# Performance work log

Hardware: AMD Instinct MI355X
Metric: run time of the kernel (lower is better)

Reference implementation:

```python
import jax, jax.numpy as jnp
import numpy as np


def gru_cell(x, h, Wih, Whh, bih, bhh):
    # torch GRU cell, gate order r, z, n
    gi = x @ Wih.T + bih
    gh = h @ Whh.T + bhh
    ir, iz, inn = jnp.split(gi, 3, axis=-1)
    hr, hz, hn = jnp.split(gh, 3, axis=-1)
    r = jax.nn.sigmoid(ir + hr)
    z = jax.nn.sigmoid(iz + hz)
    n = jnp.tanh(inn + r * hn)
    return (1.0 - z) * n + z * h


def setup_inputs() -> dict:
    key = jax.random.key(0)
    ks = jax.random.split(key, 24)
    S, T, B, E, H, V = 64, 64, 32, 512, 1024, 32000
    sc_e = 1.0 / np.sqrt(E)
    sc_h = 1.0 / np.sqrt(H)

    def rn(i, shape, sc):
        return jax.random.normal(ks[i], shape, jnp.float32) * sc

    return {
        "src": jax.random.randint(ks[0], (S, B), 0, V),
        "trg": jax.random.randint(ks[1], (T, B), 0, V),
        "emb": rn(2, (V, E), 0.02),
        # encoder forward-direction GRU
        "Wih_f": rn(3, (3 * H, E), sc_e), "Whh_f": rn(4, (3 * H, H), sc_h),
        "bih_f": rn(5, (3 * H,), sc_h), "bhh_f": rn(6, (3 * H,), sc_h),
        # encoder backward-direction GRU
        "Wih_b": rn(7, (3 * H, E), sc_e), "Whh_b": rn(8, (3 * H, H), sc_h),
        "bih_b": rn(9, (3 * H,), sc_h), "bhh_b": rn(10, (3 * H,), sc_h),
        # attention: Linear(2H -> H) and scoring vector v
        "Wa": rn(11, (H, 2 * H), sc_h), "ba": rn(12, (H,), sc_h),
        "v": rn(13, (H,), sc_h),
        # decoder GRU: input is [embedded(E); context(H)]
        "Wih_d": rn(14, (3 * H, E + H), sc_h), "Whh_d": rn(15, (3 * H, H), sc_h),
        "bih_d": rn(16, (3 * H,), sc_h), "bhh_d": rn(17, (3 * H,), sc_h),
        # output head Linear(2H -> V)
        "Wout": rn(18, (V, 2 * H), sc_h), "bout": rn(19, (V,), sc_h),
    }


def reference(src, trg, emb, Wih_f, Whh_f, bih_f, bhh_f, Wih_b, Whh_b, bih_b, bhh_b,
              Wa, ba, v, Wih_d, Whh_d, bih_d, bhh_d, Wout, bout):
    S, B = src.shape
    H = Whh_f.shape[1]

    # ---- encoder: bidirectional GRU, fwd+bwd output halves summed ----
    src_emb = emb[src]  # [S, B, E]
    h0 = jnp.zeros((B, H), src_emb.dtype)

    def step_f(h, x):
        h2 = gru_cell(x, h, Wih_f, Whh_f, bih_f, bhh_f)
        return h2, h2

    def step_b(h, x):
        h2 = gru_cell(x, h, Wih_b, Whh_b, bih_b, bhh_b)
        return h2, h2

    h_fwd, out_f = jax.lax.scan(step_f, h0, src_emb)
    _, out_b_rev = jax.lax.scan(step_b, h0, src_emb[::-1])
    enc_out = out_f + out_b_rev[::-1]          # [S, B, H]
    enc_bt = enc_out.transpose(1, 0, 2)        # [B, S, H]

    # ---- decoder with teacher forcing (ratio fixed to 1.0) ----
    dec_tokens = jnp.concatenate([src[-1:], trg[:-1]], axis=0)  # [T, B]
    dec_emb = emb[dec_tokens]                                   # [T, B, E]

    def dec_step(h, e_t):
        # Bahdanau attention: relu(Linear([h; enc])) scored by v
        hrep = jnp.broadcast_to(h[:, None, :], enc_bt.shape)    # [B, S, H]
        energy = jax.nn.relu(jnp.concatenate([hrep, enc_bt], -1) @ Wa.T + ba)
        scores = energy @ v                                     # [B, S]
        a = jax.nn.softmax(scores, axis=1)
        ctx = jnp.einsum('bs,bsh->bh', a, enc_bt)               # [B, H]
        rnn_in = jnp.concatenate([e_t, ctx], axis=-1)           # [B, E+H]
        h_new = gru_cell(rnn_in, h, Wih_d, Whh_d, bih_d, bhh_d)
        logits = jnp.concatenate([h_new, ctx], -1) @ Wout.T + bout  # [B, V]
        return h_new, logits

    _, outputs = jax.lax.scan(dec_step, h_fwd, dec_emb)  # [T, B, V]
    return outputs
```

## Files before the change

kernel.cpp:

```cpp
#include <hip/hip_runtime.h>
#include <hip/hip_bf16.h>

#define S_ 64
#define T_ 64
#define B_ 32
#define E_ 512
#define H_ 1024
#define V_ 32000
#define H3 3072
#define H2 2048
#define EH 1536

typedef unsigned short u16;
typedef unsigned int u32;
typedef unsigned long long u64;
typedef __attribute__((ext_vector_type(8))) short bf16x8;
typedef __attribute__((ext_vector_type(4))) float f32x4;

#define MFMA3(ACC, AH_, AL_, BH_, BL_)                                              \
    ACC = __builtin_amdgcn_mfma_f32_16x16x32_bf16(AL_, BH_, ACC, 0, 0, 0);          \
    ACC = __builtin_amdgcn_mfma_f32_16x16x32_bf16(AH_, BL_, ACC, 0, 0, 0);          \
    ACC = __builtin_amdgcn_mfma_f32_16x16x32_bf16(AH_, BH_, ACC, 0, 0, 0);

__device__ __forceinline__ void splitf(float x, u16& h, u16& l) {
    u32 xb = __float_as_uint(x);
    u32 hb = (xb + 0x7FFFu + ((xb >> 16) & 1u)) & 0xFFFF0000u;
    h = (u16)(hb >> 16);
    float lf = x - __uint_as_float(hb);
    u32 lb = __float_as_uint(lf);
    l = (u16)((lb + 0x7FFFu + ((lb >> 16) & 1u)) >> 16);
}

__device__ __forceinline__ float bf2f(u16 v) { return __uint_as_float(((u32)v) << 16); }

__device__ __forceinline__ void load_lds16(const void* g, void* l) {
    __builtin_amdgcn_global_load_lds((const __attribute__((address_space(1))) u32*)g,
                                     (__attribute__((address_space(3))) u32*)l, 16, 0, 0);
}

__device__ __forceinline__ bf16x8 ld_sys16(const u16* p) {
    union { bf16x8 v; u64 q[2]; } u;
    const u64* q = (const u64*)p;
    u.q[0] = __hip_atomic_load(q,     __ATOMIC_RELAXED, __HIP_MEMORY_SCOPE_SYSTEM);
    u.q[1] = __hip_atomic_load(q + 1, __ATOMIC_RELAXED, __HIP_MEMORY_SCOPE_SYSTEM);
    return u.v;
}
__device__ __forceinline__ float ld_sysf(const float* p) {
    return __hip_atomic_load(p, __ATOMIC_RELAXED, __HIP_MEMORY_SCOPE_SYSTEM);
}
__device__ __forceinline__ void st_sysf(float* p, float v) {
    __hip_atomic_store(p, v, __ATOMIC_RELAXED, __HIP_MEMORY_SCOPE_SYSTEM);
}
__device__ __forceinline__ void st_sysu16(u16* p, u16 v) {
    __hip_atomic_store(p, v, __ATOMIC_RELAXED, __HIP_MEMORY_SCOPE_SYSTEM);
}

__device__ __forceinline__ void gbar(int* cnt, int* flag, int nblk, int blk, int& gen) {
    __syncthreads();
    if (threadIdx.x == 0) {
        gen += 1;
        asm volatile("s_waitcnt vmcnt(0)" ::: "memory");
        __hip_atomic_fetch_add(&cnt[(blk & 7) << 5], 1, __ATOMIC_RELAXED,
                               __HIP_MEMORY_SCOPE_SYSTEM);
        if (blk == 0) {
            const int target = nblk * gen;
            for (;;) {
                int sum = 0;
#pragma unroll
                for (int j = 0; j < 8; ++j)
                    sum += __hip_atomic_load(&cnt[j << 5], __ATOMIC_RELAXED,
                                             __HIP_MEMORY_SCOPE_SYSTEM);
                if (sum >= target) break;
                __builtin_amdgcn_s_sleep(2);
            }
#pragma unroll
            for (int j = 0; j < 8; ++j)
                __hip_atomic_store(&flag[j << 5], gen, __ATOMIC_RELAXED,
                                   __HIP_MEMORY_SCOPE_SYSTEM);
        } else {
            while (__hip_atomic_load(&flag[(blk & 7) << 5], __ATOMIC_RELAXED,
                                     __HIP_MEMORY_SCOPE_SYSTEM) < gen)
                __builtin_amdgcn_s_sleep(2);
        }
    }
    __syncthreads();
}

__global__ void k_embed_src_split(const int* __restrict__ src, const float* __restrict__ emb,
                                  u16* __restrict__ hi, u16* __restrict__ lo) {
    int row = blockIdx.x;
    int tok = src[row];
    int c = threadIdx.x * 4;
    float4 v = *reinterpret_cast<const float4*>(emb + (size_t)tok * E_ + c);
    ushort4 h, l;
    splitf(v.x, h.x, l.x); splitf(v.y, h.y, l.y);
    splitf(v.z, h.z, l.z); splitf(v.w, h.w, l.w);
    *reinterpret_cast<ushort4*>(hi + (size_t)row * E_ + c) = h;
    *reinterpret_cast<ushort4*>(lo + (size_t)row * E_ + c) = l;
}

__global__ void k_embed_dec_split(const int* __restrict__ src, const int* __restrict__ trg,
                                  const float* __restrict__ emb,
                                  u16* __restrict__ hi, u16* __restrict__ lo) {
    int row = blockIdx.x;
    int t = row >> 5, b = row & 31;
    int tok = (t == 0) ? src[(S_ - 1) * B_ + b] : trg[(t - 1) * B_ + b];
    int c = threadIdx.x * 4;
    float4 v = *reinterpret_cast<const float4*>(emb + (size_t)tok * E_ + c);
    ushort4 h, l;
    splitf(v.x, h.x, l.x); splitf(v.y, h.y, l.y);
    splitf(v.z, h.z, l.z); splitf(v.w, h.w, l.w);
    *reinterpret_cast<ushort4*>(hi + (size_t)row * E_ + c) = h;
    *reinterpret_cast<ushort4*>(lo + (size_t)row * E_ + c) = l;
}

__global__ __launch_bounds__(256) void k_split(const float* __restrict__ in, int ld, int cols4,
                                               u16* __restrict__ hi, u16* __restrict__ lo) {
    int c4 = blockIdx.x * 256 + threadIdx.x;
    if (c4 >= cols4) return;
    size_t r = blockIdx.y;
    float4 v = *reinterpret_cast<const float4*>(in + r * ld + (size_t)c4 * 4);
    ushort4 h, l;
    splitf(v.x, h.x, l.x); splitf(v.y, h.y, l.y);
    splitf(v.z, h.z, l.z); splitf(v.w, h.w, l.w);
    size_t o = (r * cols4 + c4) * 4;
    *reinterpret_cast<ushort4*>(hi + o) = h;
    *reinterpret_cast<ushort4*>(lo + o) = l;
}

__global__ __launch_bounds__(256) void k_split_sum_enc(
    const float* __restrict__ ef, const float* __restrict__ eb, float* __restrict__ es,
    u16* __restrict__ hi, u16* __restrict__ lo) {
    size_t r = blockIdx.y;
    int c4 = threadIdx.x * 4;
    float4 va = *reinterpret_cast<const float4*>(ef + r * H_ + c4);
    float4 vb = *reinterpret_cast<const float4*>(eb + r * H_ + c4);
    float4 v; v.x = va.x + vb.x; v.y = va.y + vb.y; v.z = va.z + vb.z; v.w = va.w + vb.w;
    *reinterpret_cast<float4*>(es + r * H_ + c4) = v;
    ushort4 h, l;
    splitf(v.x, h.x, l.x); splitf(v.y, h.y, l.y);
    splitf(v.z, h.z, l.z); splitf(v.w, h.w, l.w);
    *reinterpret_cast<ushort4*>(hi + r * H_ + c4) = h;
    *reinterpret_cast<ushort4*>(lo + r * H_ + c4) = l;
}

__global__ void k_wsplit_perm(const float* __restrict__ src, int ld, int coff,
                              u16* __restrict__ hi, u16* __restrict__ lo) {
    int r = blockIdx.x;
    int i = r / 3, g = r - i * 3;
    const float* p = src + (size_t)(g * H_ + i) * ld + coff;
    int c = threadIdx.x * 4;
    float4 v = *reinterpret_cast<const float4*>(p + c);
    ushort4 h, l;
    splitf(v.x, h.x, l.x); splitf(v.y, h.y, l.y);
    splitf(v.z, h.z, l.z); splitf(v.w, h.w, l.w);
    *reinterpret_cast<ushort4*>(hi + (size_t)r * H_ + c) = h;
    *reinterpret_cast<ushort4*>(lo + (size_t)r * H_ + c) = l;
}

__global__ __launch_bounds__(256, 2) void k_gemm_mfma3(
    const u16* __restrict__ Ah, const u16* __restrict__ Al,
    const u16* __restrict__ Bh, const u16* __restrict__ Bl,
    const float* __restrict__ bias, float* __restrict__ C,
    int ldc, int K)
{
    __shared__ u16 ls[4][128 * 32];
    const int tid = threadIdx.x;
    const int lane = tid & 63, w = tid >> 6;
    const int wr = w >> 1, wc = w & 1;
    const size_t m0 = (size_t)blockIdx.x * 128, n0 = (size_t)blockIdx.y * 128;

    const int c0 = (w * 2) * 64 + lane;
    const int r0 = c0 >> 2, kc0 = (c0 & 3) << 3;
    const size_t rstep = (size_t)16 * K;
    const u16* gAh = Ah + (m0 + r0) * K + kc0;
    const u16* gAl = Al + (m0 + r0) * K + kc0;
    const u16* gBh = Bh + (n0 + r0) * K + kc0;
    const u16* gBl = Bl + (n0 + r0) * K + kc0;
    const int lo0 = c0 * 8;

    const int frow = lane & 15, fk = (lane >> 4) << 3;
    const int offA = (wr * 64 + frow) * 32 + fk;
    const int offB = (wc * 64 + frow) * 32 + fk;

    f32x4 acc[4][4] = {};

    for (int k0 = 0; k0 < K; k0 += 32) {
        load_lds16(gAh + k0, &ls[0][lo0]);
        load_lds16(gAh + rstep + k0, &ls[0][lo0 + 512]);
        load_lds16(gAl + k0, &ls[1][lo0]);
        load_lds16(gAl + rstep + k0, &ls[1][lo0 + 512]);
        load_lds16(gBh + k0, &ls[2][lo0]);
        load_lds16(gBh + rstep + k0, &ls[2][lo0 + 512]);
        load_lds16(gBl + k0, &ls[3][lo0]);
        load_lds16(gBl + rstep + k0, &ls[3][lo0 + 512]);
        __syncthreads();

        bf16x8 fAh[4], fAl[4], fBh[4], fBl[4];
#pragma unroll
        for (int m = 0; m < 4; ++m) {
            fAh[m] = *reinterpret_cast<const bf16x8*>(&ls[0][offA + m * 512]);
            fAl[m] = *reinterpret_cast<const bf16x8*>(&ls[1][offA + m * 512]);
        }
#pragma unroll
        for (int n = 0; n < 4; ++n) {
            fBh[n] = *reinterpret_cast<const bf16x8*>(&ls[2][offB + n * 512]);
            fBl[n] = *reinterpret_cast<const bf16x8*>(&ls[3][offB + n * 512]);
        }
#pragma unroll
        for (int m = 0; m < 4; ++m)
#pragma unroll
            for (int n = 0; n < 4; ++n) {
                MFMA3(acc[m][n], fAh[m], fAl[m], fBh[n], fBl[n]);
            }
        __syncthreads();
    }

    const int crow0 = wr * 64 + ((lane >> 4) << 2);
    const int ccol0 = wc * 64 + (lane & 15);
#pragma unroll
    for (int n = 0; n < 4; ++n) {
        const size_t col = n0 + ccol0 + n * 16;
        const float bv = bias ? bias[col] : 0.f;
#pragma unroll
        for (int m = 0; m < 4; ++m)
#pragma unroll
            for (int r = 0; r < 4; ++r)
                C[(m0 + crow0 + m * 16 + r) * (size_t)ldc + col] = acc[m][n][r] + bv;
    }
}

__global__ __launch_bounds__(256) void k_enc_persist(
    const u16* __restrict__ whhf_h, const u16* __restrict__ whhf_l,
    const u16* __restrict__ whhb_h, const u16* __restrict__ whhb_l,
    const float* __restrict__ gi_f, const float* __restrict__ gi_b,
    const float* __restrict__ bhh_f, const float* __restrict__ bhh_b,
    u16* __restrict__ hfH0, u16* __restrict__ hfL0,
    u16* __restrict__ hfH1, u16* __restrict__ hfL1,
    u16* __restrict__ hbH0, u16* __restrict__ hbL0,
    u16* __restrict__ hbH1, u16* __restrict__ hbL1,
    float* __restrict__ enc_f, float* __restrict__ enc_b,
    int* __restrict__ cnt, int* __restrict__ flag)
{
    __shared__ __align__(16) char smem[145792];
    u16* lAh  = (u16*)smem;
    u16* lAl  = (u16*)(smem + 65536);
    float* ex0 = (float*)(smem + 131072);
    float* ex1 = (float*)(smem + 137408);
    float* hloc = (float*)(smem + 143744);

    const int blk = blockIdx.x, tid = threadIdx.x;
    const int lane = tid & 63, w = tid >> 6;
    const int dir = blk >> 6, c = blk & 63;
    const int i0 = c * 16;
    const u16* WH = (dir ? whhb_h : whhf_h) + (size_t)c * 48 * 1024;
    const u16* WL = (dir ? whhb_l : whhf_l) + (size_t)c * 48 * 1024;
    const float* gi = dir ? gi_b : gi_f;
    const float* bhh = dir ? bhh_b : bhh_f;
    float* encd = dir ? enc_b : enc_f;
    int gen = 0;

    for (int q = tid; q < 512; q += 256) hloc[q] = 0.f;

    const int frow = lane & 15, fk8 = (lane >> 4) << 3;
    const int cb = lane & 15, rb0 = (lane >> 4) << 2;

    for (int t = 0; t < 64; ++t) {
        const int a = t & 1;
        const u16* rH = dir ? (a ? hbH1 : hbH0) : (a ? hfH1 : hfH0);
        const u16* rL = dir ? (a ? hbL1 : hbL0) : (a ? hfL1 : hfL0);
        u16* oH = dir ? (a ? hbH0 : hbH1) : (a ? hfH0 : hfH1);
        u16* oL = dir ? (a ? hbL0 : hbL1) : (a ? hfL0 : hfL1);
        const int s = dir ? 63 - t : t;

#pragma unroll
        for (int ch0 = 0; ch0 < 4096; ch0 += 256) {
            int ch = ch0 + tid;
            int r = ch >> 7, kc = (ch & 127) << 3;
            int sw = kc ^ ((r & 7) << 3);
            *(bf16x8*)&lAh[r * 1024 + sw] = ld_sys16(&rH[r * 1024 + kc]);
            *(bf16x8*)&lAl[r * 1024 + sw] = ld_sys16(&rL[r * 1024 + kc]);
        }
        __syncthreads();

#pragma unroll
        for (int jj = 0; jj < 3; ++jj) {
            const int j = w * 3 + jj;
            const int m = j & 1;
            const int n = (j >> 1) % 3;
            const int kh = j / 6;
            const int arow = m * 16 + frow;
            const int asw = (arow & 7) << 3;
            const u16* gBh = WH + (size_t)(n * 16 + frow) * 1024;
            const u16* gBl = WL + (size_t)(n * 16 + frow) * 1024;
            f32x4 acc = {};
            const int ke = kh * 512 + 512;
#pragma unroll 4
            for (int k0 = kh * 512; k0 < ke; k0 += 32) {
                int kc = k0 + fk8;
                bf16x8 aH = *(const bf16x8*)&lAh[arow * 1024 + (kc ^ asw)];
                bf16x8 aL = *(const bf16x8*)&lAl[arow * 1024 + (kc ^ asw)];
                bf16x8 bH = *(const bf16x8*)&gBh[kc];
                bf16x8 bL = *(const bf16x8*)&gBl[kc];
                MFMA3(acc, aH, aL, bH, bL);
            }
            float* exd = kh ? ex1 : ex0;
            const int pc = n * 16 + cb;
#pragma unroll
            for (int r = 0; r < 4; ++r)
                exd[pc * 33 + m * 16 + rb0 + r] = acc[r];
        }
        __syncthreads();

        {
            const int il = tid & 15, bb = tid >> 4;
            const int i = i0 + il;
#pragma unroll
            for (int q = 0; q < 2; ++q) {
                int b = bb + q * 16;
                float ghr = ex0[(3 * il + 0) * 33 + b] + ex1[(3 * il + 0) * 33 + b] + bhh[i];
                float ghz = ex0[(3 * il + 1) * 33 + b] + ex1[(3 * il + 1) * 33 + b] + bhh[H_ + i];
                float ghn = ex0[(3 * il + 2) * 33 + b] + ex1[(3 * il + 2) * 33 + b] + bhh[2 * H_ + i];
                size_t gio = (size_t)(s * B_ + b) * H3 + i;
                float gir = gi[gio], giz = gi[gio + H_], gin = gi[gio + 2 * H_];
                float rr = 1.f / (1.f + expf(-(gir + ghr)));
                float zz = 1.f / (1.f + expf(-(giz + ghz)));
                float nn = tanhf(gin + rr * ghn);
                float hold = hloc[b * 16 + il];
                float hnew = (1.f - zz) * nn + zz * hold;
                hloc[b * 16 + il] = hnew;
                u16 hh, hl; splitf(hnew, hh, hl);
                st_sysu16(&oH[b * 1024 + i], hh);
                st_sysu16(&oL[b * 1024 + i], hl);
                encd[((size_t)b * 64 + s) * H_ + i] = hnew;
            }
        }
        gbar(cnt, flag, 128, blk, gen);
    }
}

__global__ __launch_bounds__(256) void k_dec_persist(
    const u16* __restrict__ wah, const u16* __restrict__ wal,
    const u16* __restrict__ wgh, const u16* __restrict__ wgl,
    const u16* __restrict__ wdh, const u16* __restrict__ wdl,
    const float* __restrict__ gi_e, const float* __restrict__ bhh_d,
    const float* __restrict__ ep, const float* __restrict__ vvec,
    const float* __restrict__ enc,
    u16* __restrict__ hH, u16* __restrict__ hL,
    float* __restrict__ hwa, float* __restrict__ scores,
    u16* __restrict__ ctxH, u16* __restrict__ ctxL,
    float* __restrict__ states, int* __restrict__ cnt, int* __restrict__ flag)
{
    __shared__ __align__(16) char smem[140288];
    u16* lWH  = (u16*)smem;
    u16* lWL  = (u16*)(smem + 32768);
    u16* lDH  = (u16*)(smem + 65536);
    float* lenc = (float*)(smem + 98304);
    float* ex1a = (float*)(smem + 131072);
    float* ex1b = (float*)(smem + 133120);
    float* ex2a = (float*)(smem + 135168);
    float* ex2b = (float*)(smem + 137216);
    float* aw   = (float*)(smem + 139264);
    float* hloc = (float*)(smem + 139520);

    const int bid = blockIdx.x, tid = threadIdx.x;
    const int lane = tid & 63, w = tid >> 6;
    const int frow = lane & 15, fk8 = (lane >> 4) << 3;
    const int b3 = bid >> 3, sl = bid & 7;
    int gen = 0;

    for (int ch = tid; ch < 2048; ch += 256) {
        int r = ch >> 7, kc = (ch & 127) << 3;
        int sw = kc ^ ((r & 7) << 3);
        const u16 *sH, *sL;
        if (r < 4) { sH = wah + ((size_t)bid * 4 + r) * 1024;
                     sL = wal + ((size_t)bid * 4 + r) * 1024; }
        else       { sH = wgh + ((size_t)bid * 12 + r - 4) * 1024;
                     sL = wgl + ((size_t)bid * 12 + r - 4) * 1024; }
        *(bf16x8*)&lWH[r * 1024 + sw] = *(const bf16x8*)&sH[kc];
        *(bf16x8*)&lWL[r * 1024 + sw] = *(const bf16x8*)&sL[kc];
    }
    for (int ch = tid; ch < 2048; ch += 256) {
        int r = ch >> 7, kc = (ch & 127) << 3;
        int sw = kc ^ ((r & 7) << 3);
        int rowg = (r < 12) ? bid * 12 + r : bid * 12;
        *(bf16x8*)&lDH[r * 1024 + sw] = *(const bf16x8*)&wdh[(size_t)rowg * 1024 + kc];
    }
    for (int ch = tid; ch < 2048; ch += 256) {
        int s = ch >> 5, c4 = (ch & 31) << 2;
        *(float4*)&lenc[s * 128 + c4] =
            *(const float4*)&enc[((size_t)b3 * 64 + s) * 1024 + sl * 128 + c4];
    }
    if (tid < 128) {
        int b = tid >> 2, u = bid * 4 + (tid & 3);
        hloc[tid] = bf2f(hH[b * 1024 + u]) + bf2f(hL[b * 1024 + u]);
    }
    float vreg[16];
#pragma unroll
    for (int i = 0; i < 16; ++i) vreg[i] = vvec[lane + i * 64];
    __syncthreads();

    const int mt = w & 1, kh = w >> 1;
    const int bsw = (frow & 7) << 3;
    const int rowg = (frow < 12) ? bid * 12 + frow : bid * 12;
    const u16* gDl = wdl + (size_t)rowg * 1024;
    const int exw = (mt * 16 + ((lane >> 4) << 2)) * 16 + frow;

    for (int t = 0; t < 64; ++t) {
        {
            float* exA = kh ? ex1b : ex1a;
            f32x4 acc = {};
            const int ar0 = (mt * 16 + frow) * 1024;
            const int ke = kh * 512 + 512;
#pragma unroll 4
            for (int k0 = kh * 512; k0 < ke; k0 += 32) {
                int kc = k0 + fk8;
                bf16x8 aH = ld_sys16(&hH[ar0 + kc]);
                bf16x8 aL = ld_sys16(&hL[ar0 + kc]);
                bf16x8 bH = *(const bf16x8*)&lWH[frow * 1024 + (kc ^ bsw)];
                bf16x8 bL = *(const bf16x8*)&lWL[frow * 1024 + (kc ^ bsw)];
                MFMA3(acc, aH, aL, bH, bL);
            }
#pragma unroll
            for (int r = 0; r < 4; ++r) exA[exw + r * 16] = acc[r];
        }
        __syncthreads();
        if (tid < 128) {
            int b = tid >> 2, col = tid & 3;
            st_sysf(&hwa[b * 1024 + bid * 4 + col],
                    ex1a[b * 16 + col] + ex1b[b * 16 + col]);
        }
        gbar(cnt, flag, 256, bid, gen);

#pragma unroll
        for (int q2 = 0; q2 < 2; ++q2) {
            int s = sl * 8 + w * 2 + q2;
            const float* epr = ep + ((size_t)b3 * 64 + s) * 1024;
            const float* hr = hwa + b3 * 1024;
            float a2 = 0.f;
#pragma unroll
            for (int i = 0; i < 16; ++i) {
                int j = lane + i * 64;
                a2 += fmaxf(ld_sysf(&hr[j]) + epr[j], 0.f) * vreg[i];
            }
            for (int off = 32; off; off >>= 1) a2 += __shfl_down(a2, off);
            if (lane == 0) st_sysf(&scores[b3 * 64 + s], a2);
        }
        gbar(cnt, flag, 256, bid, gen);

        if (tid < 64) {
            float sc = ld_sysf(&scores[b3 * 64 + tid]);
            float m = sc;
            for (int off = 32; off; off >>= 1) m = fmaxf(m, __shfl_xor(m, off));
            float e = expf(sc - m);
            float sum = e;
            for (int off = 32; off; off >>= 1) sum += __shfl_xor(sum, off);
            aw[tid] = e / sum;
        }
        __syncthreads();
        if (tid < 128) {
            int c = tid;
            float x = 0.f;
#pragma unroll 8
            for (int s = 0; s < 64; ++s) x += aw[s] * lenc[s * 128 + c];
            states[((size_t)t * 32 + b3) * 2048 + 1024 + sl * 128 + c] = x;
            u16 hh, hl; splitf(x, hh, hl);
            st_sysu16(&ctxH[b3 * 1024 + sl * 128 + c], hh);
            st_sysu16(&ctxL[b3 * 1024 + sl * 128 + c], hl);
        }
        gbar(cnt, flag, 256, bid, gen);

        {
            float* exD = kh ? ex2b : ex2a;
            f32x4 acc = {};
            const int ar0 = (mt * 16 + frow) * 1024;
            const int ke = kh * 512 + 512;
#pragma unroll 4
            for (int k0 = kh * 512; k0 < ke; k0 += 32) {
                int kc = k0 + fk8;
                bf16x8 aH = ld_sys16(&ctxH[ar0 + kc]);
                bf16x8 aL = ld_sys16(&ctxL[ar0 + kc]);
                bf16x8 bH = *(const bf16x8*)&lDH[frow * 1024 + (kc ^ bsw)];
                bf16x8 bL = *(const bf16x8*)&gDl[kc];
                MFMA3(acc, aH, aL, bH, bL);
            }
#pragma unroll
            for (int r = 0; r < 4; ++r) exD[exw + r * 16] = acc[r];
        }
        __syncthreads();
        if (tid < 128) {
            int b = tid >> 2, ui = tid & 3;
            int u = bid * 4 + ui;
            float gicr = ex2a[b * 16 + 3 * ui + 0] + ex2b[b * 16 + 3 * ui + 0];
            float gicz = ex2a[b * 16 + 3 * ui + 1] + ex2b[b * 16 + 3 * ui + 1];
            float gicn = ex2a[b * 16 + 3 * ui + 2] + ex2b[b * 16 + 3 * ui + 2];
            float ghr = ex1a[b * 16 + 4 + 3 * ui + 0] + ex1b[b * 16 + 4 + 3 * ui + 0] + bhh_d[u];
            float ghz = ex1a[b * 16 + 4 + 3 * ui + 1] + ex1b[b * 16 + 4 + 3 * ui + 1] + bhh_d[H_ + u];
            float ghn = ex1a[b * 16 + 4 + 3 * ui + 2] + ex1b[b * 16 + 4 + 3 * ui + 2] + bhh_d[2 * H_ + u];
            size_t ge = ((size_t)t * 32 + b) * 3072;
            float gir = gi_e[ge + u] + gicr;
            float giz = gi_e[ge + 1024 + u] + gicz;
            float gin = gi_e[ge + 2048 + u] + gicn;
            float rr = 1.f / (1.f + expf(-(gir + ghr)));
            float zz = 1.f / (1.f + expf(-(giz + ghz)));
            float nn = tanhf(gin + rr * ghn);
            float hold = hloc[tid];
            float hnew = (1.f - zz) * nn + zz * hold;
            hloc[tid] = hnew;
            u16 hh, hl; splitf(hnew, hh, hl);
            st_sysu16(&hH[b * 1024 + u], hh);
            st_sysu16(&hL[b * 1024 + u], hl);
            states[((size_t)t * 32 + b) * 2048 + u] = hnew;
        }
        gbar(cnt, flag, 256, bid, gen);
    }
}

extern "C" void kernel_launch(void* const* d_in, const int* in_sizes, int n_in,
                              void* d_out, int out_size, void* d_ws, size_t ws_size,
                              hipStream_t stream) {
    const int*   src   = (const int*)d_in[0];
    const int*   trg   = (const int*)d_in[1];
    const float* emb   = (const float*)d_in[2];
    const float* Wih_f = (const float*)d_in[3];
    const float* Whh_f = (const float*)d_in[4];
    const float* bih_f = (const float*)d_in[5];
    const float* bhh_f = (const float*)d_in[6];
    const float* Wih_b = (const float*)d_in[7];
    const float* Whh_b = (const float*)d_in[8];
    const float* bih_b = (const float*)d_in[9];
    const float* bhh_b = (const float*)d_in[10];
    const float* Wa    = (const float*)d_in[11];
    const float* ba    = (const float*)d_in[12];
    const float* vv    = (const float*)d_in[13];
    const float* Wih_d = (const float*)d_in[14];
    const float* Whh_d = (const float*)d_in[15];
    const float* bih_d = (const float*)d_in[16];
    const float* bhh_d = (const float*)d_in[17];
    const float* Wout  = (const float*)d_in[18];
    const float* bout  = (const float*)d_in[19];
    float* out = (float*)d_out;
    (void)in_sizes; (void)n_in; (void)out_size; (void)ws_size;

    float* w = (float*)d_ws;
    size_t o = 0;
    auto alloc = [&](size_t n) { float* p = w + o; o += n; return p; };
    float* gi_f  = alloc((size_t)S_ * B_ * H3);
    float* gi_b  = alloc((size_t)S_ * B_ * H3);
    float* enc_f = alloc((size_t)B_ * S_ * H_);
    float* enc_b = alloc((size_t)B_ * S_ * H_);
    float* enc   = alloc((size_t)B_ * S_ * H_);
    float* ep    = alloc((size_t)B_ * S_ * H_);
    float* hwa   = alloc((size_t)B_ * H_);
    float* scores = alloc(B_ * S_);
    float* barf  = alloc(1024);
    int* cntE  = (int*)barf;
    int* flagE = cntE + 256;
    int* cntD  = cntE + 512;
    int* flagD = cntE + 768;
    float* gi_e   = gi_f;
    float* states = gi_b;

    u16* wu = (u16*)(w + o);
    size_t ou = 0;
    auto alloc16 = [&](size_t n) { u16* p = wu + ou; ou += n; return p; };
    u16* semb_h  = alloc16((size_t)S_ * B_ * E_);  u16* semb_l  = alloc16((size_t)S_ * B_ * E_);
    u16* demb_h  = alloc16((size_t)T_ * B_ * E_);  u16* demb_l  = alloc16((size_t)T_ * B_ * E_);
    u16* wihf_h  = alloc16((size_t)H3 * E_);       u16* wihf_l  = alloc16((size_t)H3 * E_);
    u16* wihb_h  = alloc16((size_t)H3 * E_);       u16* wihb_l  = alloc16((size_t)H3 * E_);
    u16* wihd_h  = alloc16((size_t)H3 * E_);       u16* wihd_l  = alloc16((size_t)H3 * E_);
    u16* wae_h   = alloc16((size_t)H_ * H_);       u16* wae_l   = alloc16((size_t)H_ * H_);
    u16* enc_h   = alloc16((size_t)B_ * S_ * H_);  u16* enc_l   = alloc16((size_t)B_ * S_ * H_);
    u16* st_h    = alloc16((size_t)T_ * B_ * H2);  u16* st_l    = alloc16((size_t)T_ * B_ * H2);
    u16* wout_h  = alloc16((size_t)6400 * H2);     u16* wout_l  = alloc16((size_t)6400 * H2);
    u16* whhf_h  = alloc16((size_t)H3 * H_);       u16* whhf_l  = alloc16((size_t)H3 * H_);
    u16* whhb_h  = alloc16((size_t)H3 * H_);       u16* whhb_l  = alloc16((size_t)H3 * H_);
    u16* wgh     = alloc16((size_t)H3 * H_);       u16* wgl     = alloc16((size_t)H3 * H_);
    u16* wdh     = alloc16((size_t)H3 * H_);       u16* wdl     = alloc16((size_t)H3 * H_);
    u16* wah     = alloc16((size_t)H_ * H_);       u16* wal     = alloc16((size_t)H_ * H_);
    u16* hsf_h[2] = {alloc16(B_ * H_), alloc16(B_ * H_)};
    u16* hsf_l[2] = {alloc16(B_ * H_), alloc16(B_ * H_)};
    u16* hsb_h[2] = {alloc16(B_ * H_), alloc16(B_ * H_)};
    u16* hsb_l[2] = {alloc16(B_ * H_), alloc16(B_ * H_)};
    u16* ctx_h   = alloc16(B_ * H_);               u16* ctx_l   = alloc16(B_ * H_);

    hipMemsetAsync(barf, 0, 1024 * sizeof(float), stream);
    hipMemsetAsync(hsf_h[0], 0, B_ * H_ * sizeof(u16), stream);
    hipMemsetAsync(hsf_l[0], 0, B_ * H_ * sizeof(u16), stream);
    hipMemsetAsync(hsb_h[0], 0, B_ * H_ * sizeof(u16), stream);
    hipMemsetAsync(hsb_l[0], 0, B_ * H_ * sizeof(u16), stream);

    k_embed_src_split<<<S_ * B_, 128, 0, stream>>>(src, emb, semb_h, semb_l);
    k_embed_dec_split<<<T_ * B_, 128, 0, stream>>>(src, trg, emb, demb_h, demb_l);

    k_split<<<dim3(1, H3), 256, 0, stream>>>(Wih_f, E_, E_ / 4, wihf_h, wihf_l);
    k_split<<<dim3(1, H3), 256, 0, stream>>>(Wih_b, E_, E_ / 4, wihb_h, wihb_l);
    k_split<<<dim3(1, H3), 256, 0, stream>>>(Wih_d, EH, E_ / 4, wihd_h, wihd_l);
    k_split<<<dim3(1, H_), 256, 0, stream>>>(Wa + H_, H2, H_ / 4, wae_h, wae_l);
    k_split<<<dim3(1, H_), 256, 0, stream>>>(Wa, H2, H_ / 4, wah, wal);
    k_wsplit_perm<<<H3, 256, 0, stream>>>(Whh_f, H_, 0, whhf_h, whhf_l);
    k_wsplit_perm<<<H3, 256, 0, stream>>>(Whh_b, H_, 0, whhb_h, whhb_l);
    k_wsplit_perm<<<H3, 256, 0, stream>>>(Whh_d, H_, 0, wgh, wgl);
    k_wsplit_perm<<<H3, 256, 0, stream>>>(Wih_d, EH, E_, wdh, wdl);

    k_gemm_mfma3<<<dim3(16, 24), 256, 0, stream>>>(semb_h, semb_l, wihf_h, wihf_l,
                                                   bih_f, gi_f, H3, E_);
    k_gemm_mfma3<<<dim3(16, 24), 256, 0, stream>>>(semb_h, semb_l, wihb_h, wihb_l,
                                                   bih_b, gi_b, H3, E_);

    k_enc_persist<<<128, 256, 0, stream>>>(
        whhf_h, whhf_l, whhb_h, whhb_l, gi_f, gi_b, bhh_f, bhh_b,
        hsf_h[0], hsf_l[0], hsf_h[1], hsf_l[1],
        hsb_h[0], hsb_l[0], hsb_h[1], hsb_l[1],
        enc_f, enc_b, cntE, flagE);

    k_split_sum_enc<<<dim3(1, B_ * S_), 256, 0, stream>>>(enc_f, enc_b, enc, enc_h, enc_l);
    k_gemm_mfma3<<<dim3(16, 8), 256, 0, stream>>>(enc_h, enc_l, wae_h, wae_l,
                                                  ba, ep, H_, H_);
    k_gemm_mfma3<<<dim3(16, 24), 256, 0, stream>>>(demb_h, demb_l, wihd_h, wihd_l,
                                                   bih_d, gi_e, H3, E_);

    k_dec_persist<<<256, 256, 0, stream>>>(
        wah, wal, wgh, wgl, wdh, wdl, gi_e, bhh_d, ep, vv, enc,
        hsf_h[0], hsf_l[0], hwa, scores, ctx_h, ctx_l, states, cntD, flagD);

    k_split<<<dim3(2, T_ * B_), 256, 0, stream>>>(states, H2, H2 / 4, st_h, st_l);
    for (int p = 0; p < 5; ++p) {
        k_split<<<dim3(2, 6400), 256, 0, stream>>>(Wout + (size_t)p * 6400 * H2, H2,
                                                   H2 / 4, wout_h, wout_l);
        k_gemm_mfma3<<<dim3(16, 50), 256, 0, stream>>>(st_h, st_l, wout_h, wout_l,
                                                       bout + p * 6400,
                                                       out + (size_t)p * 6400, V_, H2);
    }
}
```

Baseline: 4.354 ms.

## Halve decoder persistent grid and fuse attention per batch to drop grid barriers

The persistent decoder kernel goes from 256 to 128 blocks, each owning 8 hidden units (twice the weight rows). Only the hi halves of the weights stay in LDS and the lo halves are streamed from global. Attention scoring, softmax and the context reduction are now done by one owner block per batch row instead of being spread across blocks, so two grid-wide barriers per timestep collapse into one. The cost is serialized attention work in 32 owner blocks, idle non-owner blocks, and more global traffic for the lo weights and the encoder outputs, which are no longer cached in LDS.

```diff
diff --git a/kernel.cpp b/kernel.cpp
--- a/kernel.cpp
+++ b/kernel.cpp
@@ -53,6 +53,10 @@
 }
 __device__ __forceinline__ void st_sysu16(u16* p, u16 v) {
     __hip_atomic_store(p, v, __ATOMIC_RELAXED, __HIP_MEMORY_SCOPE_SYSTEM);
+}
+__device__ __forceinline__ void st_sys64(u16* p, ushort4 v) {
+    union { ushort4 s; u64 q; } u; u.s = v;
+    __hip_atomic_store((u64*)p, u.q, __ATOMIC_RELAXED, __HIP_MEMORY_SCOPE_SYSTEM);
 }
 
 __device__ __forceinline__ void gbar(int* cnt, int* flag, int nblk, int blk, int& gen) {
@@ -347,52 +351,41 @@
     const float* __restrict__ ep, const float* __restrict__ vvec,
     const float* __restrict__ enc,
     u16* __restrict__ hH, u16* __restrict__ hL,
-    float* __restrict__ hwa, float* __restrict__ scores,
+    float* __restrict__ hwa,
     u16* __restrict__ ctxH, u16* __restrict__ ctxL,
     float* __restrict__ states, int* __restrict__ cnt, int* __restrict__ flag)
 {
-    __shared__ __align__(16) char smem[140288];
-    u16* lWH  = (u16*)smem;
-    u16* lWL  = (u16*)(smem + 32768);
-    u16* lDH  = (u16*)(smem + 65536);
-    float* lenc = (float*)(smem + 98304);
-    float* ex1a = (float*)(smem + 131072);
-    float* ex1b = (float*)(smem + 133120);
-    float* ex2a = (float*)(smem + 135168);
-    float* ex2b = (float*)(smem + 137216);
-    float* aw   = (float*)(smem + 139264);
-    float* hloc = (float*)(smem + 139520);
+    __shared__ __align__(16) char smem[123648];
+    u16* lWH   = (u16*)smem;
+    u16* lDH   = (u16*)(smem + 65536);
+    float* ex1 = (float*)(smem + 114688);
+    float* ex2 = (float*)(smem + 118912);
+    float* al  = (float*)(smem + 122080);
+    float* aw  = (float*)(smem + 122336);
+    float* hloc = (float*)(smem + 122592);
 
     const int bid = blockIdx.x, tid = threadIdx.x;
     const int lane = tid & 63, w = tid >> 6;
     const int frow = lane & 15, fk8 = (lane >> 4) << 3;
-    const int b3 = bid >> 3, sl = bid & 7;
+    const bool owner = (bid & 3) == 0;
+    const int b3 = bid >> 2;
     int gen = 0;
 
-    for (int ch = tid; ch < 2048; ch += 256) {
+    for (int ch = tid; ch < 4096; ch += 256) {
         int r = ch >> 7, kc = (ch & 127) << 3;
         int sw = kc ^ ((r & 7) << 3);
-        const u16 *sH, *sL;
-        if (r < 4) { sH = wah + ((size_t)bid * 4 + r) * 1024;
-                     sL = wal + ((size_t)bid * 4 + r) * 1024; }
-        else       { sH = wgh + ((size_t)bid * 12 + r - 4) * 1024;
-                     sL = wgl + ((size_t)bid * 12 + r - 4) * 1024; }
-        *(bf16x8*)&lWH[r * 1024 + sw] = *(const bf16x8*)&sH[kc];
-        *(bf16x8*)&lWL[r * 1024 + sw] = *(const bf16x8*)&sL[kc];
-    }
-    for (int ch = tid; ch < 2048; ch += 256) {
+        const u16* s = (r < 8) ? wah + ((size_t)(bid * 8 + r)) * 1024
+                               : wgh + ((size_t)(bid * 24 + r - 8)) * 1024;
+        *(bf16x8*)&lWH[r * 1024 + sw] = *(const bf16x8*)&s[kc];
+    }
+    for (int ch = tid; ch < 3072; ch += 256) {
         int r = ch >> 7, kc = (ch & 127) << 3;
         int sw = kc ^ ((r & 7) << 3);
-        int rowg = (r < 12) ? bid * 12 + r : bid * 12;
-        *(bf16x8*)&lDH[r * 1024 + sw] = *(const bf16x8*)&wdh[(size_t)rowg * 1024 + kc];
-    }
-    for (int ch = tid; ch < 2048; ch += 256) {
-        int s = ch >> 5, c4 = (ch & 31) << 2;
-        *(float4*)&lenc[s * 128 + c4] =
-            *(const float4*)&enc[((size_t)b3 * 64 + s) * 1024 + sl * 128 + c4];
-    }
-    if (tid < 128) {
-        int b = tid >> 2, u = bid * 4 + (tid & 3);
+        *(bf16x8*)&lDH[r * 1024 + sw] =
+            *(const bf16x8*)&wdh[((size_t)(bid * 24 + r)) * 1024 + kc];
+    }
+    {
+        int b = tid >> 3, u = bid * 8 + (tid & 7);
         hloc[tid] = bf2f(hH[b * 1024 + u]) + bf2f(hL[b * 1024 + u]);
     }
     float vreg[16];
@@ -400,103 +393,117 @@
     for (int i = 0; i < 16; ++i) vreg[i] = vvec[lane + i * 64];
     __syncthreads();
 
-    const int mt = w & 1, kh = w >> 1;
-    const int bsw = (frow & 7) << 3;
-    const int rowg = (frow < 12) ? bid * 12 + frow : bid * 12;
-    const u16* gDl = wdl + (size_t)rowg * 1024;
-    const int exw = (mt * 16 + ((lane >> 4) << 2)) * 16 + frow;
+    const int m = w & 1, n = w >> 1;
+    const int cb = lane & 15, rb0 = (lane >> 4) << 2;
 
     for (int t = 0; t < 64; ++t) {
         {
-            float* exA = kh ? ex1b : ex1a;
+            const int arow = m * 16 + frow;
+            const int lrB = n * 16 + frow;
+            const int bsw = (lrB & 7) << 3;
+            const u16* gBl = (lrB < 8) ? wal + ((size_t)(bid * 8 + lrB)) * 1024
+                                       : wgl + ((size_t)(bid * 24 + lrB - 8)) * 1024;
             f32x4 acc = {};
-            const int ar0 = (mt * 16 + frow) * 1024;
-            const int ke = kh * 512 + 512;
 #pragma unroll 4
-            for (int k0 = kh * 512; k0 < ke; k0 += 32) {
+            for (int k0 = 0; k0 < 1024; k0 += 32) {
                 int kc = k0 + fk8;
-                bf16x8 aH = ld_sys16(&hH[ar0 + kc]);
-                bf16x8 aL = ld_sys16(&hL[ar0 + kc]);
-                bf16x8 bH = *(const bf16x8*)&lWH[frow * 1024 + (kc ^ bsw)];
-                bf16x8 bL = *(const bf16x8*)&lWL[frow * 1024 + (kc ^ bsw)];
+                bf16x8 aH = ld_sys16(&hH[arow * 1024 + kc]);
+                bf16x8 aL = ld_sys16(&hL[arow * 1024 + kc]);
+                bf16x8 bH = *(const bf16x8*)&lWH[lrB * 1024 + (kc ^ bsw)];
+                bf16x8 bL = *(const bf16x8*)&gBl[kc];
                 MFMA3(acc, aH, aL, bH, bL);
             }
-#pragma unroll
-            for (int r = 0; r < 4; ++r) exA[exw + r * 16] = acc[r];
+            const int pc = n * 16 + cb;
+#pragma unroll
+            for (int r = 0; r < 4; ++r)
+                ex1[pc * 33 + m * 16 + rb0 + r] = acc[r];
         }
         __syncthreads();
-        if (tid < 128) {
-            int b = tid >> 2, col = tid & 3;
-            st_sysf(&hwa[b * 1024 + bid * 4 + col],
-                    ex1a[b * 16 + col] + ex1b[b * 16 + col]);
-        }
-        gbar(cnt, flag, 256, bid, gen);
-
-#pragma unroll
-        for (int q2 = 0; q2 < 2; ++q2) {
-            int s = sl * 8 + w * 2 + q2;
-            const float* epr = ep + ((size_t)b3 * 64 + s) * 1024;
-            const float* hr = hwa + b3 * 1024;
-            float a2 = 0.f;
-#pragma unroll
-            for (int i = 0; i < 16; ++i) {
-                int j = lane + i * 64;
-                a2 += fmaxf(ld_sysf(&hr[j]) + epr[j], 0.f) * vreg[i];
-            }
-            for (int off = 32; off; off >>= 1) a2 += __shfl_down(a2, off);
-            if (lane == 0) st_sysf(&scores[b3 * 64 + s], a2);
-        }
-        gbar(cnt, flag, 256, bid, gen);
-
-        if (tid < 64) {
-            float sc = ld_sysf(&scores[b3 * 64 + tid]);
-            float m = sc;
-            for (int off = 32; off; off >>= 1) m = fmaxf(m, __shfl_xor(m, off));
-            float e = expf(sc - m);
-            float sum = e;
-            for (int off = 32; off; off >>= 1) sum += __shfl_xor(sum, off);
-            aw[tid] = e / sum;
+        {
+            int b = tid >> 3, cc = tid & 7;
+            st_sysf(&hwa[b * 1024 + bid * 8 + cc], ex1[cc * 33 + b]);
+        }
+        gbar(cnt, flag, 128, bid, gen);
+
+        if (owner) {
+            float hreg[16];
+#pragma unroll
+            for (int i = 0; i < 16; ++i)
+                hreg[i] = ld_sysf(&hwa[b3 * 1024 + lane + i * 64]);
+            for (int ii = 0; ii < 16; ++ii) {
+                int s = w * 16 + ii;
+                const float* epr = ep + ((size_t)b3 * 64 + s) * 1024;
+                float a2 = 0.f;
+#pragma unroll
+                for (int i = 0; i < 16; ++i) {
+                    int j = lane + i * 64;
+                    a2 += fmaxf(hreg[i] + epr[j], 0.f) * vreg[i];
+                }
+                for (int off = 32; off; off >>= 1) a2 += __shfl_down(a2, off);
+                if (lane == 0) al[s] = a2;
+            }
+            __syncthreads();
+            if (tid < 64) {
+                float sc = al[tid];
+                float mx = sc;
+                for (int off = 32; off; off >>= 1) mx = fmaxf(mx, __shfl_xor(mx, off));
+                float e = expf(sc - mx);
+                float sum = e;
+                for (int off = 32; off; off >>= 1) sum += __shfl_xor(sum, off);
+                aw[tid] = e / sum;
+            }
+            __syncthreads();
+            {
+                int c4 = tid * 4;
+                float4 x = {0.f, 0.f, 0.f, 0.f};
+                for (int s = 0; s < 64; ++s) {
+                    float a = aw[s];
+                    float4 e4 = *(const float4*)&enc[((size_t)b3 * 64 + s) * 1024 + c4];
+                    x.x += a * e4.x; x.y += a * e4.y; x.z += a * e4.z; x.w += a * e4.w;
+                }
+                *(float4*)&states[((size_t)t * 32 + b3) * 2048 + 1024 + c4] = x;
+                ushort4 chh, cll;
+                splitf(x.x, chh.x, cll.x); splitf(x.y, chh.y, cll.y);
+                splitf(x.z, chh.z, cll.z); splitf(x.w, chh.w, cll.w);
+                st_sys64(&ctxH[b3 * 1024 + c4], chh);
+                st_sys64(&ctxL[b3 * 1024 + c4], cll);
+            }
+        }
+        gbar(cnt, flag, 128, bid, gen);
+
+        {
+            const int rbase = n * 8;
+            const int lrB = rbase + frow;
+            const int bsw = (lrB & 7) << 3;
+            const u16* gBl = wdl + ((size_t)(bid * 24 + lrB)) * 1024;
+            const int arow = m * 16 + frow;
+            f32x4 acc = {};
+#pragma unroll 4
+            for (int k0 = 0; k0 < 1024; k0 += 32) {
+                int kc = k0 + fk8;
+                bf16x8 aH = ld_sys16(&ctxH[arow * 1024 + kc]);
+                bf16x8 aL = ld_sys16(&ctxL[arow * 1024 + kc]);
+                bf16x8 bH = *(const bf16x8*)&lDH[lrB * 1024 + (kc ^ bsw)];
+                bf16x8 bL = *(const bf16x8*)&gBl[kc];
+                MFMA3(acc, aH, aL, bH, bL);
+            }
+            if (n == 0 || cb >= 8) {
+                const int pc = rbase + cb;
+#pragma unroll
+                for (int r = 0; r < 4; ++r)
+                    ex2[pc * 33 + m * 16 + rb0 + r] = acc[r];
+            }
         }
         __syncthreads();
-        if (tid < 128) {
-            int c = tid;
-            float x = 0.f;
-#pragma unroll 8
-            for (int s = 0; s < 64; ++s) x += aw[s] * lenc[s * 128 + c];
-            states[((size_t)t * 32 + b3) * 2048 + 1024 + sl * 128 + c] = x;
-            u16 hh, hl; splitf(x, hh, hl);
-            st_sysu16(&ctxH[b3 * 1024 + sl * 128 + c], hh);
-            st_sysu16(&ctxL[b3 * 1024 + sl * 128 + c], hl);
-        }
-        gbar(cnt, flag, 256, bid, gen);
-
         {
-            float* exD = kh ? ex2b : ex2a;
-            f32x4 acc = {};
-            const int ar0 = (mt * 16 + frow) * 1024;
-            const int ke = kh * 512 + 512;
-#pragma unroll 4
-            for (int k0 = kh * 512; k0 < ke; k0 += 32) {
-                int kc = k0 + fk8;
-                bf16x8 aH = ld_sys16(&ctxH[ar0 + kc]);
-                bf16x8 aL = ld_sys16(&ctxL[ar0 + kc]);
-                bf16x8 bH = *(const bf16x8*)&lDH[frow * 1024 + (kc ^ bsw)];
-                bf16x8 bL = *(const bf16x8*)&gDl[kc];
-                MFMA3(acc, aH, aL, bH, bL);
-            }
-#pragma unroll
-            for (int r = 0; r < 4; ++r) exD[exw + r * 16] = acc[r];
-        }
-        __syncthreads();
-        if (tid < 128) {
-            int b = tid >> 2, ui = tid & 3;
-            int u = bid * 4 + ui;
-            float gicr = ex2a[b * 16 + 3 * ui + 0] + ex2b[b * 16 + 3 * ui + 0];
-            float gicz = ex2a[b * 16 + 3 * ui + 1] + ex2b[b * 16 + 3 * ui + 1];
-            float gicn = ex2a[b * 16 + 3 * ui + 2] + ex2b[b * 16 + 3 * ui + 2];
-            float ghr = ex1a[b * 16 + 4 + 3 * ui + 0] + ex1b[b * 16 + 4 + 3 * ui + 0] + bhh_d[u];
-            float ghz = ex1a[b * 16 + 4 + 3 * ui + 1] + ex1b[b * 16 + 4 + 3 * ui + 1] + bhh_d[H_ + u];
-            float ghn = ex1a[b * 16 + 4 + 3 * ui + 2] + ex1b[b * 16 + 4 + 3 * ui + 2] + bhh_d[2 * H_ + u];
+            int b = tid >> 3, ui = tid & 7;
+            int u = bid * 8 + ui;
+            float gicr = ex2[(3 * ui + 0) * 33 + b];
+            float gicz = ex2[(3 * ui + 1) * 33 + b];
+            float gicn = ex2[(3 * ui + 2) * 33 + b];
+            float ghr = ex1[(8 + 3 * ui + 0) * 33 + b] + bhh_d[u];
+            float ghz = ex1[(8 + 3 * ui + 1) * 33 + b] + bhh_d[H_ + u];
+            float ghn = ex1[(8 + 3 * ui + 2) * 33 + b] + bhh_d[2 * H_ + u];
             size_t ge = ((size_t)t * 32 + b) * 3072;
             float gir = gi_e[ge + u] + gicr;
             float giz = gi_e[ge + 1024 + u] + gicz;
@@ -512,7 +519,7 @@
             st_sysu16(&hL[b * 1024 + u], hl);
             states[((size_t)t * 32 + b) * 2048 + u] = hnew;
         }
-        gbar(cnt, flag, 256, bid, gen);
+        gbar(cnt, flag, 128, bid, gen);
     }
 }
 
@@ -552,7 +559,6 @@
     float* enc   = alloc((size_t)B_ * S_ * H_);
     float* ep    = alloc((size_t)B_ * S_ * H_);
     float* hwa   = alloc((size_t)B_ * H_);
-    float* scores = alloc(B_ * S_);
     float* barf  = alloc(1024);
     int* cntE  = (int*)barf;
     int* flagE = cntE + 256;
@@ -620,9 +626,9 @@
     k_gemm_mfma3<<<dim3(16, 24), 256, 0, stream>>>(demb_h, demb_l, wihd_h, wihd_l,
                                                    bih_d, gi_e, H3, E_);
 
-    k_dec_persist<<<256, 256, 0, stream>>>(
+    k_dec_persist<<<128, 256, 0, stream>>>(
         wah, wal, wgh, wgl, wdh, wdl, gi_e, bhh_d, ep, vv, enc,
-        hsf_h[0], hsf_l[0], hwa, scores, ctx_h, ctx_l, states, cntD, flagD);
+        hsf_h[0], hsf_l[0], hwa, ctx_h, ctx_l, states, cntD, flagD);
 
     k_split<<<dim3(2, T_ * B_), 256, 0, stream>>>(states, H2, H2 / 4, st_h, st_l);
     for (int p = 0; p < 5; ++p) {
```

Result: slower. 9.396 ms (+115.8%).
